# Kernel tuning notes

Measured on AMD Instinct MI355X. Metric: run time of the kernel, lower is better.

Reference implementation:

```python
import jax, jax.numpy as jnp
import numpy as np

H = 1024

def setup_inputs() -> dict:
    key = jax.random.key(0)
    ks = jax.random.split(key, 9)
    s = 1.0 / np.sqrt(H)
    x = jax.random.normal(ks[0], (4, 2048, H), dtype=jnp.float32)
    Wq = jax.random.uniform(ks[1], (H, H), jnp.float32, -s, s)
    bq = jax.random.uniform(ks[2], (H,), jnp.float32, -s, s)
    Wk = jax.random.uniform(ks[3], (H, H), jnp.float32, -s, s)
    bk = jax.random.uniform(ks[4], (H,), jnp.float32, -s, s)
    Wv = jax.random.uniform(ks[5], (H, H), jnp.float32, -s, s)
    bv = jax.random.uniform(ks[6], (H,), jnp.float32, -s, s)
    Wo = jax.random.uniform(ks[7], (H, H), jnp.float32, -s, s)
    bo = jax.random.uniform(ks[8], (H,), jnp.float32, -s, s)
    return {"x": x, "Wq": Wq, "bq": bq, "Wk": Wk, "bk": bk,
            "Wv": Wv, "bv": bv, "Wo": Wo, "bo": bo}

def reference(x, Wq, bq, Wk, bk, Wv, bv, Wo, bo):
    # Linear uses y = x @ W.T + b (torch convention: W is [out, in])
    q = jnp.einsum('bsd,ed->bse', x, Wq) + bq
    k = jnp.einsum('bsd,ed->bse', x, Wk) + bk
    v = jnp.einsum('bsd,ed->bse', x, Wv) + bv
    scale = q.shape[-1] ** 0.5
    attn = jnp.einsum('bqe,bke->bqk', q, k) / scale  # [B,S,S]
    attn = jax.nn.softmax(attn, axis=-1)
    out = jnp.einsum('bqk,bke->bqe', attn, v)
    return jnp.einsum('bse,oe->bso', out, Wo) + bo
```

## Files before the change

### kernel.cpp

```cpp
#include <hip/hip_runtime.h>

typedef short  short4v __attribute__((ext_vector_type(4)));
typedef short  short8v __attribute__((ext_vector_type(8)));
typedef __bf16 bf16x8  __attribute__((ext_vector_type(8)));
typedef float  f32x4   __attribute__((ext_vector_type(4)));
typedef float  float4v __attribute__((ext_vector_type(4)));

__device__ __forceinline__ short f2bf(float f) {
  unsigned u = __builtin_bit_cast(unsigned, f);
  u += 0x7fffu + ((u >> 16) & 1u);
  return (short)(u >> 16);
}
__device__ __forceinline__ float bf2f(short h) {
  unsigned u = ((unsigned)(unsigned short)h) << 16;
  return __builtin_bit_cast(float, u);
}
__device__ __forceinline__ bf16x8 ld8(const short* p) {
  return __builtin_bit_cast(bf16x8, *reinterpret_cast<const short8v*>(p));
}

__constant__ const float kExpScale = 0.04508422f;

__global__ __launch_bounds__(256) void k_cvt(const float* __restrict__ in,
                                             short* __restrict__ out) {
  const int i = blockIdx.x * 256 + threadIdx.x;
#pragma unroll
  for (int j = 0; j < 4; ++j) {
    const long g = (long)i + (long)j * 524288;
    float4v v = *reinterpret_cast<const float4v*>(in + g * 4);
    short4v o;
    o[0] = f2bf(v[0]); o[1] = f2bf(v[1]); o[2] = f2bf(v[2]); o[3] = f2bf(v[3]);
    *reinterpret_cast<short4v*>(out + g * 4) = o;
  }
}

__global__ __launch_bounds__(256) void k_wprep(const float* __restrict__ i0,
    const float* __restrict__ i1, const float* __restrict__ i2,
    const float* __restrict__ i3, short* __restrict__ o0, short* __restrict__ o1,
    short* __restrict__ o2, short* __restrict__ o3) {
  const int z = blockIdx.z;
  const float* in = z == 0 ? i0 : z == 1 ? i1 : z == 2 ? i2 : i3;
  short* out = z == 0 ? o0 : z == 1 ? o1 : z == 2 ? o2 : o3;
  const float sc = (z == 1) ? kExpScale : 1.0f;
  const int tid = threadIdx.x;
  const int c0 = blockIdx.x << 6;
  const int r0 = blockIdx.y << 7;
  if (z == 3) {
#pragma unroll
    for (int j = 0; j < 8; ++j) {
      int idx = j * 256 + tid;
      int r = idx >> 4, c4 = (idx & 15) << 2;
      float4v v = *reinterpret_cast<const float4v*>(in + (long)(r0 + r) * 1024 + c0 + c4);
      short4v o;
      o[0] = f2bf(v[0]); o[1] = f2bf(v[1]); o[2] = f2bf(v[2]); o[3] = f2bf(v[3]);
      *reinterpret_cast<short4v*>(out + (long)(r0 + r) * 1024 + c0 + c4) = o;
    }
    return;
  }
  __shared__ float tile[128][65];
#pragma unroll
  for (int j = 0; j < 8; ++j) {
    int idx = j * 256 + tid;
    int r = idx >> 4, c4 = (idx & 15) << 2;
    float4v v = *reinterpret_cast<const float4v*>(in + (long)(r0 + r) * 1024 + c0 + c4);
    tile[r][c4 + 0] = v[0] * sc; tile[r][c4 + 1] = v[1] * sc;
    tile[r][c4 + 2] = v[2] * sc; tile[r][c4 + 3] = v[3] * sc;
  }
  __syncthreads();
#pragma unroll
  for (int j = 0; j < 8; ++j) {
    int idx = j * 256 + tid;
    int rO = idx >> 5, g4 = (idx & 31) << 2;
    short4v o;
    o[0] = f2bf(tile[g4 + 0][rO]); o[1] = f2bf(tile[g4 + 1][rO]);
    o[2] = f2bf(tile[g4 + 2][rO]); o[3] = f2bf(tile[g4 + 3][rO]);
    *reinterpret_cast<short4v*>(out + (long)(c0 + rO) * 1024 + r0 + g4) = o;
  }
}

__device__ __forceinline__ void gemm_loop(const short* __restrict__ Ab,
    const short* __restrict__ Bb, int K, int lda, int ldb, int bm, int bn,
    f32x4 (&acc)[4][4]) {
  __shared__ __align__(16) short lsA[128 * 64];
  __shared__ __align__(16) short lsB[128 * 64];
  const int tid = threadIdx.x;
  const int lane = tid & 63, wid = tid >> 6;
  const int wr = wid >> 1, wc = wid & 1;
  const int fr = lane & 15, fq = lane >> 4;
  for (int kt = 0; kt < K; kt += 64) {
    __syncthreads();
#pragma unroll
    for (int c = 0; c < 4; ++c) {
      const int idx = c * 256 + tid;
      const int row = idx >> 3, colh = (idx & 7) << 3;
      const short* ga = Ab + (long)(bm + row) * lda + kt + colh;
      const short* gb = Bb + (long)(bn + row) * ldb + kt + colh;
      __builtin_amdgcn_global_load_lds(
          (const __attribute__((address_space(1))) void*)ga,
          (__attribute__((address_space(3))) void*)&lsA[idx * 8], 16, 0, 0);
      __builtin_amdgcn_global_load_lds(
          (const __attribute__((address_space(1))) void*)gb,
          (__attribute__((address_space(3))) void*)&lsB[idx * 8], 16, 0, 0);
    }
    __syncthreads();
#pragma unroll
    for (int ks = 0; ks < 64; ks += 32) {
      bf16x8 a[4], b[4];
#pragma unroll
      for (int m = 0; m < 4; ++m)
        a[m] = ld8(&lsA[(wr * 64 + m * 16 + fr) * 64 + ks + fq * 8]);
#pragma unroll
      for (int n = 0; n < 4; ++n)
        b[n] = ld8(&lsB[(wc * 64 + n * 16 + fr) * 64 + ks + fq * 8]);
#pragma unroll
      for (int m = 0; m < 4; ++m)
#pragma unroll
        for (int n = 0; n < 4; ++n)
          acc[m][n] = __builtin_amdgcn_mfma_f32_16x16x32_bf16(a[m], b[n], acc[m][n], 0, 0, 0);
    }
  }
}

__global__ __launch_bounds__(256, 3) void k_prep2(
    const short* __restrict__ wkT, const short* __restrict__ wqT,
    const short* __restrict__ wob, const short* __restrict__ wvT,
    const float* __restrict__ bq, const float* __restrict__ Wo,
    const float* __restrict__ bv,
    short* __restrict__ mt, short* __restrict__ wv2,
    float* __restrict__ bvec, float* __restrict__ bvp) {
  const int tid = threadIdx.x;
  const int lane = tid & 63, wid = tid >> 6;
  if (blockIdx.z == 2) {
    const int r0 = (blockIdx.y * 8 + blockIdx.x) * 16;
#pragma unroll
    for (int rr = 0; rr < 4; ++rr) {
      const int row = r0 + wid * 4 + rr;
      {
        const short* xr = wkT + (long)row * 1024 + lane * 16;
        short8v a0 = *reinterpret_cast<const short8v*>(xr);
        short8v a1 = *reinterpret_cast<const short8v*>(xr + 8);
        float s = 0.f;
#pragma unroll
        for (int j = 0; j < 8; ++j) s += bf2f(a0[j]) * bq[lane * 16 + j];
#pragma unroll
        for (int j = 0; j < 8; ++j) s += bf2f(a1[j]) * bq[lane * 16 + 8 + j];
#pragma unroll
        for (int off = 32; off; off >>= 1) s += __shfl_xor(s, off);
        if (lane == 0) bvec[row] = s * kExpScale;
      }
      {
        float s = 0.f;
#pragma unroll
        for (int j = 0; j < 16; ++j)
          s += Wo[(long)row * 1024 + j * 64 + lane] * bv[j * 64 + lane];
#pragma unroll
        for (int off = 32; off; off >>= 1) s += __shfl_xor(s, off);
        if (lane == 0) bvp[row] = s;
      }
    }
    return;
  }
  const short* A = blockIdx.z == 0 ? wkT : wob;
  const short* B = blockIdx.z == 0 ? wqT : wvT;
  short* C = blockIdx.z == 0 ? mt : wv2;
  const int bm = blockIdx.x * 128, bn = blockIdx.y * 128;
  f32x4 acc[4][4] = {};
  gemm_loop(A, B, 1024, 1024, 1024, bm, bn, acc);
  const int wr = wid >> 1, wc = wid & 1;
  const int fr = lane & 15, fq = lane >> 4;
#pragma unroll
  for (int n = 0; n < 4; ++n) {
    const int col = bn + wc * 64 + n * 16 + fr;
#pragma unroll
    for (int m = 0; m < 4; ++m) {
      const int row0 = bm + wr * 64 + m * 16 + fq * 4;
#pragma unroll
      for (int i = 0; i < 4; ++i)
        C[(long)(row0 + i) * 1024 + col] = f2bf(acc[m][n][i]);
    }
  }
}

template <int MODE>
__global__ __launch_bounds__(256, 3) void k_gemm(
    const short* __restrict__ A, const short* __restrict__ B,
    const float* __restrict__ b0p, float* __restrict__ b1p,
    void* __restrict__ C0,
    int K, int lda, int ldb, long sA, long sB, long sC, int ldC) {
  __shared__ float invL[128];
  const int tid = threadIdx.x;
  const int lane = tid & 63, wid = tid >> 6;
  const int wr = wid >> 1, wc = wid & 1;
  const int fr = lane & 15, fq = lane >> 4;
  const int bm = blockIdx.x * 128, bn = blockIdx.y * 128;
  const int bz = blockIdx.z;

  if constexpr (MODE == 4) {
    const int row = tid >> 1, half = tid & 1;
    const float* pr = b1p + ((long)bz * 2048 + bm + row) * 32 + half * 16;
    float s = 0.f;
#pragma unroll
    for (int j = 0; j < 4; ++j) {
      float4v v = *reinterpret_cast<const float4v*>(pr + j * 4);
      s += v[0] + v[1] + v[2] + v[3];
    }
    s += __shfl_xor(s, 1);
    if (half == 0) invL[row] = 1.0f / s;
  }

  f32x4 acc[4][4] = {};
  gemm_loop(A + (long)bz * sA, B + (long)bz * sB, K, lda, ldb, bm, bn, acc);

  if constexpr (MODE == 3) {
    short* O = (short*)C0 + (long)bz * sC;
    float wv[4];
#pragma unroll
    for (int n = 0; n < 4; ++n)
      wv[n] = b0p[(long)bz * 2048 + bn + wc * 64 + n * 16 + fr];
#pragma unroll
    for (int m = 0; m < 4; ++m) {
#pragma unroll
      for (int i = 0; i < 4; ++i) {
        const int row = bm + wr * 64 + m * 16 + fq * 4 + i;
        float rs = 0.f;
#pragma unroll
        for (int n = 0; n < 4; ++n) {
          float e = exp2f(acc[m][n][i] + wv[n]);
          O[(long)row * ldC + bn + wc * 64 + n * 16 + fr] = f2bf(e);
          rs += e;
        }
        rs += __shfl_xor(rs, 1); rs += __shfl_xor(rs, 2);
        rs += __shfl_xor(rs, 4); rs += __shfl_xor(rs, 8);
        if (fr == 0)
          b1p[((long)bz * 2048 + row) * 32 + (blockIdx.y << 1) + wc] = rs;
      }
    }
  } else {
#pragma unroll
    for (int n = 0; n < 4; ++n) {
      const int coll = wc * 64 + n * 16 + fr;
#pragma unroll
      for (int m = 0; m < 4; ++m) {
        const int rl0 = wr * 64 + m * 16 + fq * 4;
#pragma unroll
        for (int i = 0; i < 4; ++i) {
          const long row = bm + rl0 + i, col = bn + coll;
          float* O = (float*)C0 + (long)bz * sC;
          O[row * ldC + col] = acc[m][n][i] * invL[rl0 + i] + b0p[col];
        }
      }
    }
  }
}

__global__ __launch_bounds__(256, 3) void k_gemmTV(
    const short* __restrict__ xb, const short* __restrict__ mt,
    const short* __restrict__ wv2, const float* __restrict__ bvp,
    const float* __restrict__ bvec, short* __restrict__ T,
    short* __restrict__ vTp, float* __restrict__ w8) {
  const int tid = threadIdx.x;
  const int lane = tid & 63, wid = tid >> 6;
  if (blockIdx.z == 2) {
    const int rbase = (blockIdx.x * 8 + blockIdx.y) * 16;
#pragma unroll
    for (int rr = 0; rr < 4; ++rr) {
      const int row = rbase + wid * 4 + rr;
      const short* xr = xb + (long)row * 1024 + lane * 16;
      short8v a0 = *reinterpret_cast<const short8v*>(xr);
      short8v a1 = *reinterpret_cast<const short8v*>(xr + 8);
      float s = 0.f;
#pragma unroll
      for (int j = 0; j < 8; ++j) s += bf2f(a0[j]) * bvec[lane * 16 + j];
#pragma unroll
      for (int j = 0; j < 8; ++j) s += bf2f(a1[j]) * bvec[lane * 16 + 8 + j];
#pragma unroll
      for (int off = 32; off; off >>= 1) s += __shfl_xor(s, off);
      if (lane == 0) w8[row] = s;
    }
    return;
  }
  const short *A, *B; const float* bias; short* C; int ldC, bm, bn;
  if (blockIdx.z == 0) {
    A = xb; B = mt; bias = nullptr; C = T; ldC = 1024;
    bm = blockIdx.x * 128; bn = blockIdx.y * 128;
  } else {
    A = wv2; B = xb; bias = bvp; C = vTp; ldC = 8192;
    bm = blockIdx.y * 128; bn = blockIdx.x * 128;
  }
  f32x4 acc[4][4] = {};
  gemm_loop(A, B, 1024, 1024, 1024, bm, bn, acc);
  const int wr = wid >> 1, wc = wid & 1;
  const int fr = lane & 15, fq = lane >> 4;
#pragma unroll
  for (int n = 0; n < 4; ++n) {
    const int col = bn + wc * 64 + n * 16 + fr;
#pragma unroll
    for (int m = 0; m < 4; ++m) {
      const int row0 = bm + wr * 64 + m * 16 + fq * 4;
#pragma unroll
      for (int i = 0; i < 4; ++i) {
        const float bvr = bias ? bias[row0 + i] : 0.f;
        C[(long)(row0 + i) * ldC + col] = f2bf(acc[m][n][i] + bvr);
      }
    }
  }
}

extern "C" void kernel_launch(void* const* d_in, const int* in_sizes, int n_in,
                              void* d_out, int out_size, void* d_ws, size_t ws_size,
                              hipStream_t stream) {
  const float* x  = (const float*)d_in[0];
  const float* Wq = (const float*)d_in[1];
  const float* bq = (const float*)d_in[2];
  const float* Wk = (const float*)d_in[3];
  const float* Wv = (const float*)d_in[5];
  const float* bv = (const float*)d_in[6];
  const float* Wo = (const float*)d_in[7];
  const float* bo = (const float*)d_in[8];

  char* ws = (char*)d_ws;
  short* xb   = (short*)ws; ws += 8192L * 1024 * 2;
  short* wkT  = (short*)ws; ws += 1024L * 1024 * 2;
  short* wob  = (short*)ws; ws += 1024L * 1024 * 2;
  short* wqT  = (short*)ws; ws += 1024L * 1024 * 2;
  short* wvT  = (short*)ws; ws += 1024L * 1024 * 2;
  short* mt   = (short*)ws; ws += 1024L * 1024 * 2;
  short* wv2  = (short*)ws; ws += 1024L * 1024 * 2;
  short* T    = (short*)ws; ws += 8192L * 1024 * 2;
  short* vTp  = (short*)ws; ws += 1024L * 8192 * 2;
  short* Sc   = (short*)ws; ws += 4L * 2048 * 2048 * 2;
  float* psum = (float*)ws; ws += 4L * 2048 * 32 * 4;
  float* w8   = (float*)ws; ws += 8192L * 4;
  float* bvec = (float*)ws; ws += 1024L * 4;
  float* bvp  = (float*)ws; ws += 1024L * 4;

  dim3 b256(256);
  k_cvt<<<2048, b256, 0, stream>>>(x, xb);
  k_wprep<<<dim3(16, 8, 4), b256, 0, stream>>>(
      Wk, Wq, Wv, Wo, wkT, wqT, wvT, wob);
  k_prep2<<<dim3(8, 8, 3), b256, 0, stream>>>(
      wkT, wqT, wob, wvT, bq, Wo, bv, mt, wv2, bvec, bvp);
  k_gemmTV<<<dim3(64, 8, 3), b256, 0, stream>>>(
      xb, mt, wv2, bvp, bvec, T, vTp, w8);
  k_gemm<3><<<dim3(16, 16, 4), b256, 0, stream>>>(
      T, xb, w8, psum, Sc,
      1024, 1024, 1024, 2048L * 1024, 2048L * 1024, 2048L * 2048, 2048);
  k_gemm<4><<<dim3(16, 8, 4), b256, 0, stream>>>(
      Sc, vTp, bo, psum, (float*)d_out,
      2048, 2048, 8192, 2048L * 2048, 2048, 2048L * 1024, 1024);
}
```

Measured before the change: 197.9 us.

## Replace attention GEMMs with larger-tile double-buffered LDS-DMA kernel

Replaces the 128x128 k_gemm used for the score/exp GEMM and the PV/output GEMM with a 512-thread kernel using 256x256 or 128x256 tiles. Operand tiles are double-buffered in LDS via global_load_lds direct loads, so the next K-slice is fetched while the current one is multiplied. Larger tiles raise arithmetic intensity and cut global traffic, but use much more LDS (about 192KB at BM=256), which lowers occupancy and may fail or spill if it exceeds the LDS budget. There is no LDS swizzle, so the fragment reads may hit bank conflicts.

After: 196.2 us. About the same (-0.9%).

```diff
diff --git a/kernel.cpp b/kernel.cpp
--- a/kernel.cpp
+++ b/kernel.cpp
@@ -181,78 +181,6 @@
   }
 }
 
-template <int MODE>
-__global__ __launch_bounds__(256, 3) void k_gemm(
-    const short* __restrict__ A, const short* __restrict__ B,
-    const float* __restrict__ b0p, float* __restrict__ b1p,
-    void* __restrict__ C0,
-    int K, int lda, int ldb, long sA, long sB, long sC, int ldC) {
-  __shared__ float invL[128];
-  const int tid = threadIdx.x;
-  const int lane = tid & 63, wid = tid >> 6;
-  const int wr = wid >> 1, wc = wid & 1;
-  const int fr = lane & 15, fq = lane >> 4;
-  const int bm = blockIdx.x * 128, bn = blockIdx.y * 128;
-  const int bz = blockIdx.z;
-
-  if constexpr (MODE == 4) {
-    const int row = tid >> 1, half = tid & 1;
-    const float* pr = b1p + ((long)bz * 2048 + bm + row) * 32 + half * 16;
-    float s = 0.f;
-#pragma unroll
-    for (int j = 0; j < 4; ++j) {
-      float4v v = *reinterpret_cast<const float4v*>(pr + j * 4);
-      s += v[0] + v[1] + v[2] + v[3];
-    }
-    s += __shfl_xor(s, 1);
-    if (half == 0) invL[row] = 1.0f / s;
-  }
-
-  f32x4 acc[4][4] = {};
-  gemm_loop(A + (long)bz * sA, B + (long)bz * sB, K, lda, ldb, bm, bn, acc);
-
-  if constexpr (MODE == 3) {
-    short* O = (short*)C0 + (long)bz * sC;
-    float wv[4];
-#pragma unroll
-    for (int n = 0; n < 4; ++n)
-      wv[n] = b0p[(long)bz * 2048 + bn + wc * 64 + n * 16 + fr];
-#pragma unroll
-    for (int m = 0; m < 4; ++m) {
-#pragma unroll
-      for (int i = 0; i < 4; ++i) {
-        const int row = bm + wr * 64 + m * 16 + fq * 4 + i;
-        float rs = 0.f;
-#pragma unroll
-        for (int n = 0; n < 4; ++n) {
-          float e = exp2f(acc[m][n][i] + wv[n]);
-          O[(long)row * ldC + bn + wc * 64 + n * 16 + fr] = f2bf(e);
-          rs += e;
-        }
-        rs += __shfl_xor(rs, 1); rs += __shfl_xor(rs, 2);
-        rs += __shfl_xor(rs, 4); rs += __shfl_xor(rs, 8);
-        if (fr == 0)
-          b1p[((long)bz * 2048 + row) * 32 + (blockIdx.y << 1) + wc] = rs;
-      }
-    }
-  } else {
-#pragma unroll
-    for (int n = 0; n < 4; ++n) {
-      const int coll = wc * 64 + n * 16 + fr;
-#pragma unroll
-      for (int m = 0; m < 4; ++m) {
-        const int rl0 = wr * 64 + m * 16 + fq * 4;
-#pragma unroll
-        for (int i = 0; i < 4; ++i) {
-          const long row = bm + rl0 + i, col = bn + coll;
-          float* O = (float*)C0 + (long)bz * sC;
-          O[row * ldC + col] = acc[m][n][i] * invL[rl0 + i] + b0p[col];
-        }
-      }
-    }
-  }
-}
-
 __global__ __launch_bounds__(256, 3) void k_gemmTV(
     const short* __restrict__ xb, const short* __restrict__ mt,
     const short* __restrict__ wv2, const float* __restrict__ bvp,
@@ -301,6 +229,131 @@
       for (int i = 0; i < 4; ++i) {
         const float bvr = bias ? bias[row0 + i] : 0.f;
         C[(long)(row0 + i) * ldC + col] = f2bf(acc[m][n][i] + bvr);
+      }
+    }
+  }
+}
+
+template <int BM, int MODE>
+__global__ __launch_bounds__(512, 2) void k2ph(
+    const short* __restrict__ A, const short* __restrict__ B,
+    const float* __restrict__ b0p, float* __restrict__ b1p,
+    void* __restrict__ C0,
+    int K, int lda, int ldb, long sA, long sB, long sC, int ldC) {
+  constexpr int MFR = BM / 32;
+  __shared__ __align__(16) short lsA[2][BM * 64];
+  __shared__ __align__(16) short lsB[2][256 * 64];
+  __shared__ float invL[128];
+  const int tid = threadIdx.x;
+  const int lane = tid & 63, wid = tid >> 6;
+  const int wr = wid >> 2, wc = wid & 3;
+  const int fr = lane & 15, fq = lane >> 4;
+  const int bm = blockIdx.x * BM, bn = blockIdx.y * 256;
+  const int bz = blockIdx.z;
+  const short* Ab = A + (long)bz * sA;
+  const short* Bb = B + (long)bz * sB;
+  const int nt = K >> 6;
+
+  if constexpr (MODE == 4) {
+    if (tid < 256) {
+      const int row = tid >> 1, half = tid & 1;
+      const float* pr = b1p + ((long)bz * 2048 + bm + row) * 32 + half * 16;
+      float s = 0.f;
+#pragma unroll
+      for (int j = 0; j < 4; ++j) {
+        float4v v = *reinterpret_cast<const float4v*>(pr + j * 4);
+        s += v[0] + v[1] + v[2] + v[3];
+      }
+      s += __shfl_xor(s, 1);
+      if (half == 0) invL[row] = 1.0f / s;
+    }
+  }
+
+  auto stage = [&](int buf, int kt) {
+#pragma unroll
+    for (int c = 0; c < BM / 64; ++c) {
+      const int idx = c * 512 + tid;
+      const int row = idx >> 3, colh = (idx & 7) << 3;
+      __builtin_amdgcn_global_load_lds(
+          (const __attribute__((address_space(1))) void*)
+              (Ab + (long)(bm + row) * lda + kt + colh),
+          (__attribute__((address_space(3))) void*)&lsA[buf][idx * 8], 16, 0, 0);
+    }
+#pragma unroll
+    for (int c = 0; c < 4; ++c) {
+      const int idx = c * 512 + tid;
+      const int row = idx >> 3, colh = (idx & 7) << 3;
+      __builtin_amdgcn_global_load_lds(
+          (const __attribute__((address_space(1))) void*)
+              (Bb + (long)(bn + row) * ldb + kt + colh),
+          (__attribute__((address_space(3))) void*)&lsB[buf][idx * 8], 16, 0, 0);
+    }
+  };
+
+  f32x4 acc[MFR][4] = {};
+
+  stage(0, 0);
+  __syncthreads();
+  for (int t = 0; t < nt; ++t) {
+    const int cur = t & 1;
+    if (t + 1 < nt) stage(cur ^ 1, (t + 1) << 6);
+    const short* cA = lsA[cur];
+    const short* cB = lsB[cur];
+#pragma unroll
+    for (int ks = 0; ks < 64; ks += 32) {
+      bf16x8 a[MFR], b[4];
+#pragma unroll
+      for (int m = 0; m < MFR; ++m)
+        a[m] = ld8(&cA[(wr * (BM / 2) + m * 16 + fr) * 64 + ks + fq * 8]);
+#pragma unroll
+      for (int n = 0; n < 4; ++n)
+        b[n] = ld8(&cB[(wc * 64 + n * 16 + fr) * 64 + ks + fq * 8]);
+#pragma unroll
+      for (int m = 0; m < MFR; ++m)
+#pragma unroll
+        for (int n = 0; n < 4; ++n)
+          acc[m][n] = __builtin_amdgcn_mfma_f32_16x16x32_bf16(a[m], b[n], acc[m][n], 0, 0, 0);
+    }
+    __syncthreads();
+  }
+
+  if constexpr (MODE == 3) {
+    short* O = (short*)C0 + (long)bz * sC;
+    float wv[4];
+#pragma unroll
+    for (int n = 0; n < 4; ++n)
+      wv[n] = b0p[(long)bz * 2048 + bn + wc * 64 + n * 16 + fr];
+#pragma unroll
+    for (int m = 0; m < MFR; ++m) {
+#pragma unroll
+      for (int i = 0; i < 4; ++i) {
+        const int row = bm + wr * (BM / 2) + m * 16 + fq * 4 + i;
+        float rs = 0.f;
+#pragma unroll
+        for (int n = 0; n < 4; ++n) {
+          float e = exp2f(acc[m][n][i] + wv[n]);
+          O[(long)row * ldC + bn + wc * 64 + n * 16 + fr] = f2bf(e);
+          rs += e;
+        }
+        rs += __shfl_xor(rs, 1); rs += __shfl_xor(rs, 2);
+        rs += __shfl_xor(rs, 4); rs += __shfl_xor(rs, 8);
+        if (fr == 0)
+          b1p[((long)bz * 2048 + row) * 32 + (bn >> 6) + wc] = rs;
+      }
+    }
+  } else {
+#pragma unroll
+    for (int n = 0; n < 4; ++n) {
+      const int coll = wc * 64 + n * 16 + fr;
+#pragma unroll
+      for (int m = 0; m < MFR; ++m) {
+        const int rl0 = wr * (BM / 2) + m * 16 + fq * 4;
+#pragma unroll
+        for (int i = 0; i < 4; ++i) {
+          const long row = bm + rl0 + i, col = bn + coll;
+          float* O = (float*)C0 + (long)bz * sC;
+          O[row * ldC + col] = acc[m][n][i] * invL[rl0 + i] + b0p[col];
+        }
       }
     }
   }
@@ -334,7 +387,7 @@
   float* bvec = (float*)ws; ws += 1024L * 4;
   float* bvp  = (float*)ws; ws += 1024L * 4;
 
-  dim3 b256(256);
+  dim3 b256(256), b512(512);
   k_cvt<<<2048, b256, 0, stream>>>(x, xb);
   k_wprep<<<dim3(16, 8, 4), b256, 0, stream>>>(
       Wk, Wq, Wv, Wo, wkT, wqT, wvT, wob);
@@ -342,10 +395,10 @@
       wkT, wqT, wob, wvT, bq, Wo, bv, mt, wv2, bvec, bvp);
   k_gemmTV<<<dim3(64, 8, 3), b256, 0, stream>>>(
       xb, mt, wv2, bvp, bvec, T, vTp, w8);
-  k_gemm<3><<<dim3(16, 16, 4), b256, 0, stream>>>(
+  k2ph<256, 3><<<dim3(8, 8, 4), b512, 0, stream>>>(
       T, xb, w8, psum, Sc,
       1024, 1024, 1024, 2048L * 1024, 2048L * 1024, 2048L * 2048, 2048);
-  k_gemm<4><<<dim3(16, 8, 4), b256, 0, stream>>>(
+  k2ph<128, 4><<<dim3(16, 4, 4), b512, 0, stream>>>(
       Sc, vTp, bo, psum, (float*)d_out,
       2048, 2048, 8192, 2048L * 2048, 2048, 2048L * 1024, 1024);
 }
```

## Use 128x256 tiles with 512 threads for scores GEMM

Applied to the files above, without the earlier changes.

The scores GEMM gets its own kernel: 512 threads with 8 waves in a 2x4 layout, each block computing a 128x256 output tile. Each block loads a 64-deep K slice into LDS through global_load_lds, so the A tile is shared across twice as many output columns. The goal is less global and L2 traffic per FLOP and half as many blocks. In exchange the kernel is single-buffered with two barriers per K step, and the larger LDS footprint may lower occupancy. The partial-sum indexing is updated to match: 8 column blocks of 4 waves each fill the 32 slots.

New measurement: 187.7 us. 5.2% less time.

```diff
diff --git a/kernel.cpp b/kernel.cpp
--- a/kernel.cpp
+++ b/kernel.cpp
@@ -181,78 +181,6 @@
   }
 }
 
-template <int MODE>
-__global__ __launch_bounds__(256, 3) void k_gemm(
-    const short* __restrict__ A, const short* __restrict__ B,
-    const float* __restrict__ b0p, float* __restrict__ b1p,
-    void* __restrict__ C0,
-    int K, int lda, int ldb, long sA, long sB, long sC, int ldC) {
-  __shared__ float invL[128];
-  const int tid = threadIdx.x;
-  const int lane = tid & 63, wid = tid >> 6;
-  const int wr = wid >> 1, wc = wid & 1;
-  const int fr = lane & 15, fq = lane >> 4;
-  const int bm = blockIdx.x * 128, bn = blockIdx.y * 128;
-  const int bz = blockIdx.z;
-
-  if constexpr (MODE == 4) {
-    const int row = tid >> 1, half = tid & 1;
-    const float* pr = b1p + ((long)bz * 2048 + bm + row) * 32 + half * 16;
-    float s = 0.f;
-#pragma unroll
-    for (int j = 0; j < 4; ++j) {
-      float4v v = *reinterpret_cast<const float4v*>(pr + j * 4);
-      s += v[0] + v[1] + v[2] + v[3];
-    }
-    s += __shfl_xor(s, 1);
-    if (half == 0) invL[row] = 1.0f / s;
-  }
-
-  f32x4 acc[4][4] = {};
-  gemm_loop(A + (long)bz * sA, B + (long)bz * sB, K, lda, ldb, bm, bn, acc);
-
-  if constexpr (MODE == 3) {
-    short* O = (short*)C0 + (long)bz * sC;
-    float wv[4];
-#pragma unroll
-    for (int n = 0; n < 4; ++n)
-      wv[n] = b0p[(long)bz * 2048 + bn + wc * 64 + n * 16 + fr];
-#pragma unroll
-    for (int m = 0; m < 4; ++m) {
-#pragma unroll
-      for (int i = 0; i < 4; ++i) {
-        const int row = bm + wr * 64 + m * 16 + fq * 4 + i;
-        float rs = 0.f;
-#pragma unroll
-        for (int n = 0; n < 4; ++n) {
-          float e = exp2f(acc[m][n][i] + wv[n]);
-          O[(long)row * ldC + bn + wc * 64 + n * 16 + fr] = f2bf(e);
-          rs += e;
-        }
-        rs += __shfl_xor(rs, 1); rs += __shfl_xor(rs, 2);
-        rs += __shfl_xor(rs, 4); rs += __shfl_xor(rs, 8);
-        if (fr == 0)
-          b1p[((long)bz * 2048 + row) * 32 + (blockIdx.y << 1) + wc] = rs;
-      }
-    }
-  } else {
-#pragma unroll
-    for (int n = 0; n < 4; ++n) {
-      const int coll = wc * 64 + n * 16 + fr;
-#pragma unroll
-      for (int m = 0; m < 4; ++m) {
-        const int rl0 = wr * 64 + m * 16 + fq * 4;
-#pragma unroll
-        for (int i = 0; i < 4; ++i) {
-          const long row = bm + rl0 + i, col = bn + coll;
-          float* O = (float*)C0 + (long)bz * sC;
-          O[row * ldC + col] = acc[m][n][i] * invL[rl0 + i] + b0p[col];
-        }
-      }
-    }
-  }
-}
-
 __global__ __launch_bounds__(256, 3) void k_gemmTV(
     const short* __restrict__ xb, const short* __restrict__ mt,
     const short* __restrict__ wv2, const float* __restrict__ bvp,
@@ -301,6 +229,132 @@
       for (int i = 0; i < 4; ++i) {
         const float bvr = bias ? bias[row0 + i] : 0.f;
         C[(long)(row0 + i) * ldC + col] = f2bf(acc[m][n][i] + bvr);
+      }
+    }
+  }
+}
+
+__global__ __launch_bounds__(512, 2) void k_scores(
+    const short* __restrict__ A, const short* __restrict__ B,
+    const float* __restrict__ b0p, float* __restrict__ b1p,
+    short* __restrict__ C0,
+    int K, long sA, long sB, long sC, int ldC) {
+  __shared__ __align__(16) short lsA[128 * 64];
+  __shared__ __align__(16) short lsB[256 * 64];
+  const int tid = threadIdx.x;
+  const int lane = tid & 63, wid = tid >> 6;
+  const int wr = wid >> 2, wc = wid & 3;
+  const int fr = lane & 15, fq = lane >> 4;
+  const int bm = blockIdx.x * 128, bn = blockIdx.y * 256;
+  const int bz = blockIdx.z;
+  const short* Ab = A + (long)bz * sA;
+  const short* Bb = B + (long)bz * sB;
+
+  f32x4 acc[4][4] = {};
+
+  for (int kt = 0; kt < K; kt += 64) {
+    __syncthreads();
+#pragma unroll
+    for (int c = 0; c < 2; ++c) {
+      const int idx = c * 512 + tid;
+      const int row = idx >> 3, colh = (idx & 7) << 3;
+      __builtin_amdgcn_global_load_lds(
+          (const __attribute__((address_space(1))) void*)
+              (Ab + (long)(bm + row) * K + kt + colh),
+          (__attribute__((address_space(3))) void*)&lsA[idx * 8], 16, 0, 0);
+    }
+#pragma unroll
+    for (int c = 0; c < 4; ++c) {
+      const int idx = c * 512 + tid;
+      const int row = idx >> 3, colh = (idx & 7) << 3;
+      __builtin_amdgcn_global_load_lds(
+          (const __attribute__((address_space(1))) void*)
+              (Bb + (long)(bn + row) * K + kt + colh),
+          (__attribute__((address_space(3))) void*)&lsB[idx * 8], 16, 0, 0);
+    }
+    __syncthreads();
+#pragma unroll
+    for (int ks = 0; ks < 64; ks += 32) {
+      bf16x8 a[4], b[4];
+#pragma unroll
+      for (int m = 0; m < 4; ++m)
+        a[m] = ld8(&lsA[(wr * 64 + m * 16 + fr) * 64 + ks + fq * 8]);
+#pragma unroll
+      for (int n = 0; n < 4; ++n)
+        b[n] = ld8(&lsB[(wc * 64 + n * 16 + fr) * 64 + ks + fq * 8]);
+#pragma unroll
+      for (int m = 0; m < 4; ++m)
+#pragma unroll
+        for (int n = 0; n < 4; ++n)
+          acc[m][n] = __builtin_amdgcn_mfma_f32_16x16x32_bf16(a[m], b[n], acc[m][n], 0, 0, 0);
+    }
+  }
+
+  short* O = C0 + (long)bz * sC;
+  float wv[4];
+#pragma unroll
+  for (int n = 0; n < 4; ++n)
+    wv[n] = b0p[(long)bz * 2048 + bn + wc * 64 + n * 16 + fr];
+#pragma unroll
+  for (int m = 0; m < 4; ++m) {
+#pragma unroll
+    for (int i = 0; i < 4; ++i) {
+      const int row = bm + wr * 64 + m * 16 + fq * 4 + i;
+      float rs = 0.f;
+#pragma unroll
+      for (int n = 0; n < 4; ++n) {
+        float e = exp2f(acc[m][n][i] + wv[n]);
+        O[(long)row * ldC + bn + wc * 64 + n * 16 + fr] = f2bf(e);
+        rs += e;
+      }
+      rs += __shfl_xor(rs, 1); rs += __shfl_xor(rs, 2);
+      rs += __shfl_xor(rs, 4); rs += __shfl_xor(rs, 8);
+      if (fr == 0)
+        b1p[((long)bz * 2048 + row) * 32 + blockIdx.y * 4 + wc] = rs;
+    }
+  }
+}
+
+__global__ __launch_bounds__(256, 3) void k_pv(
+    const short* __restrict__ A, const short* __restrict__ B,
+    const float* __restrict__ b0p, float* __restrict__ b1p,
+    float* __restrict__ C0,
+    int K, int lda, int ldb, long sA, long sB, long sC, int ldC) {
+  __shared__ float invL[128];
+  const int tid = threadIdx.x;
+  const int lane = tid & 63, wid = tid >> 6;
+  const int wr = wid >> 1, wc = wid & 1;
+  const int fr = lane & 15, fq = lane >> 4;
+  const int bm = blockIdx.x * 128, bn = blockIdx.y * 128;
+  const int bz = blockIdx.z;
+
+  {
+    const int row = tid >> 1, half = tid & 1;
+    const float* pr = b1p + ((long)bz * 2048 + bm + row) * 32 + half * 16;
+    float s = 0.f;
+#pragma unroll
+    for (int j = 0; j < 4; ++j) {
+      float4v v = *reinterpret_cast<const float4v*>(pr + j * 4);
+      s += v[0] + v[1] + v[2] + v[3];
+    }
+    s += __shfl_xor(s, 1);
+    if (half == 0) invL[row] = 1.0f / s;
+  }
+
+  f32x4 acc[4][4] = {};
+  gemm_loop(A + (long)bz * sA, B + (long)bz * sB, K, lda, ldb, bm, bn, acc);
+
+#pragma unroll
+  for (int n = 0; n < 4; ++n) {
+    const int coll = wc * 64 + n * 16 + fr;
+#pragma unroll
+    for (int m = 0; m < 4; ++m) {
+      const int rl0 = wr * 64 + m * 16 + fq * 4;
+#pragma unroll
+      for (int i = 0; i < 4; ++i) {
+        const long row = bm + rl0 + i, col = bn + coll;
+        float* O = C0 + (long)bz * sC;
+        O[row * ldC + col] = acc[m][n][i] * invL[rl0 + i] + b0p[col];
       }
     }
   }
@@ -334,7 +388,7 @@
   float* bvec = (float*)ws; ws += 1024L * 4;
   float* bvp  = (float*)ws; ws += 1024L * 4;
 
-  dim3 b256(256);
+  dim3 b256(256), b512(512);
   k_cvt<<<2048, b256, 0, stream>>>(x, xb);
   k_wprep<<<dim3(16, 8, 4), b256, 0, stream>>>(
       Wk, Wq, Wv, Wo, wkT, wqT, wvT, wob);
@@ -342,10 +396,10 @@
       wkT, wqT, wob, wvT, bq, Wo, bv, mt, wv2, bvec, bvp);
   k_gemmTV<<<dim3(64, 8, 3), b256, 0, stream>>>(
       xb, mt, wv2, bvp, bvec, T, vTp, w8);
-  k_gemm<3><<<dim3(16, 16, 4), b256, 0, stream>>>(
+  k_scores<<<dim3(16, 8, 4), b512, 0, stream>>>(
       T, xb, w8, psum, Sc,
-      1024, 1024, 1024, 2048L * 1024, 2048L * 1024, 2048L * 2048, 2048);
-  k_gemm<4><<<dim3(16, 8, 4), b256, 0, stream>>>(
+      1024, 2048L * 1024, 2048L * 1024, 2048L * 2048, 2048);
+  k_pv<<<dim3(16, 8, 4), b256, 0, stream>>>(
       Sc, vTp, bo, psum, (float*)d_out,
       2048, 2048, 8192, 2048L * 2048, 2048, 2048L * 1024, 1024);
 }
```
